# Kernel optimization log

Hardware: AMD Instinct MI355X
Metric: run time of the kernel (lower is better)

Reference implementation:

```python
import jax, jax.numpy as jnp
import numpy as np

L, D, H, F, S, B, P = 6, 1024, 16, 4096, 512, 16, 512
DH = D // H
SCALE = 1.0 / float(np.sqrt(DH))


def setup_inputs() -> dict:
    key = jax.random.key(0)
    ks = jax.random.split(key, 12)
    def n(k, shape, s=0.02):
        return jax.random.normal(k, shape, jnp.float32) * s
    x = jax.random.normal(ks[0], (B, S, D), jnp.float32)
    pe = n(ks[1], (1, P, D))                      # learnable positional encoding
    # per-layer stacked params; linear weights stored [in, out] (y = x @ W + b)
    wq = n(ks[2], (L, D, D)); wk = n(ks[3], (L, D, D)); wv = n(ks[4], (L, D, D))
    wo = n(ks[5], (L, D, D))
    bq = jnp.zeros((L, D)); bk = jnp.zeros((L, D)); bv = jnp.zeros((L, D)); bo = jnp.zeros((L, D))
    bias_table = n(ks[6], (L, 2 * P - 1, H))      # relative position bias table
    w1 = n(ks[7], (L, D, F)); b1 = jnp.zeros((L, F))
    w2 = n(ks[8], (L, F, D)); b2 = jnp.zeros((L, D))
    ln1_g = jnp.ones((L, D)); ln1_b = jnp.zeros((L, D))
    ln2_g = jnp.ones((L, D)); ln2_b = jnp.zeros((L, D))
    return dict(x=x, pe=pe, wq=wq, bq=bq, wk=wk, bk=bk, wv=wv, bv=bv, wo=wo, bo=bo,
                bias_table=bias_table, w1=w1, b1=b1, w2=w2, b2=b2,
                ln1_g=ln1_g, ln1_b=ln1_b, ln2_g=ln2_g, ln2_b=ln2_b)


def _ln(x, g, b):
    mu = jnp.mean(x, -1, keepdims=True)
    var = jnp.mean((x - mu) ** 2, -1, keepdims=True)
    return (x - mu) / jnp.sqrt(var + 1e-6) * g + b


def reference(x, pe, wq, bq, wk, bk, wv, bv, wo, bo, bias_table,
              w1, b1, w2, b2, ln1_g, ln1_b, ln2_g, ln2_b):
    idx = jnp.arange(S)
    rel = idx[:, None] - idx[None, :] + (P - 1)   # [S,S] relative position index
    h = x + pe[:, :S, :]                           # dropout is identity at eval
    for i in range(L):
        xn = _ln(h, ln1_g[i], ln1_b[i])
        q = (xn @ wq[i] + bq[i]).reshape(B, S, H, DH)
        k = (xn @ wk[i] + bk[i]).reshape(B, S, H, DH)
        v = (xn @ wv[i] + bv[i]).reshape(B, S, H, DH)
        scores = jnp.einsum('bqhd,bkhd->bhqk', q, k) * SCALE
        bias = bias_table[i][rel]                  # [S,S,H] gather
        scores = scores + jnp.transpose(bias, (2, 0, 1))[None]  # [1,H,S,S]
        aw = jax.nn.softmax(scores, axis=-1)
        ctx = jnp.einsum('bhqk,bkhd->bqhd', aw, v).reshape(B, S, D)
        attn = ctx @ wo[i] + bo[i]
        out1 = h + attn
        xn2 = _ln(out1, ln2_g[i], ln2_b[i])
        ffn = jax.nn.gelu(xn2 @ w1[i] + b1[i], approximate=False) @ w2[i] + b2[i]
        h = out1 + ffn + h                         # note: double residual, as in source
    return h
```

## Files before the change

### kernel.cpp

```cpp
#include <hip/hip_runtime.h>
#include <cstdint>

typedef unsigned short u16;
typedef __bf16 bf16x8 __attribute__((ext_vector_type(8)));
typedef unsigned short u16x8 __attribute__((ext_vector_type(8)));
typedef float f32x4 __attribute__((ext_vector_type(4)));

__device__ __forceinline__ float b2f(u16 u) { return __uint_as_float(((unsigned)u) << 16); }
__device__ __forceinline__ u16 f2b(float f) {
  unsigned u = __float_as_uint(f);
  return (u16)((u + 0x7FFFu + ((u >> 16) & 1u)) >> 16);
}

#define GLDS(g, l) __builtin_amdgcn_global_load_lds( \
    (const __attribute__((address_space(1))) void*)(g), \
    (__attribute__((address_space(3))) void*)(l), 16, 0, 0)

__global__ __launch_bounds__(256) void addpe_kernel(const float* __restrict__ x,
                                                    const float* __restrict__ pe,
                                                    float* __restrict__ h) {
  int i = blockIdx.x * 256 + threadIdx.x;
  float4 xv = ((const float4*)x)[i];
  float4 pv = ((const float4*)pe)[i & 0x1FFFF];
  float4 o;
  o.x = xv.x + pv.x; o.y = xv.y + pv.y; o.z = xv.z + pv.z; o.w = xv.w + pv.w;
  ((float4*)h)[i] = o;
}

__global__ __launch_bounds__(256) void copy_kernel(const float* __restrict__ h,
                                                   float* __restrict__ out) {
  int i = blockIdx.x * 256 + threadIdx.x;
  ((float4*)out)[i] = ((const float4*)h)[i];
}

__global__ __launch_bounds__(256) void bias_concat_kernel(const float* __restrict__ a,
                                                          const float* __restrict__ b,
                                                          const float* __restrict__ c,
                                                          float* __restrict__ o) {
  int i = blockIdx.x * 256 + threadIdx.x;
  float v = (i < 1024) ? a[i] : ((i < 2048) ? b[i - 1024] : c[i - 2048]);
  o[i] = v;
}

__global__ __launch_bounds__(256) void ln_kernel(const float* __restrict__ in,
                                                 const float* __restrict__ g,
                                                 const float* __restrict__ bta,
                                                 u16* __restrict__ out) {
  int row = blockIdx.x, t = threadIdx.x;
  const float4 v = ((const float4*)(in + (size_t)row * 1024))[t];
  float s = v.x + v.y + v.z + v.w;
  float s2 = v.x * v.x + v.y * v.y + v.z * v.z + v.w * v.w;
#pragma unroll
  for (int off = 32; off > 0; off >>= 1) { s += __shfl_xor(s, off); s2 += __shfl_xor(s2, off); }
  __shared__ __align__(16) float red[8];
  int w = t >> 6;
  if ((t & 63) == 0) { red[w] = s; red[4 + w] = s2; }
  __syncthreads();
  s = red[0] + red[1] + red[2] + red[3];
  s2 = red[4] + red[5] + red[6] + red[7];
  float mu = s * (1.0f / 1024.0f);
  float var = s2 * (1.0f / 1024.0f) - mu * mu;
  float rstd = rsqrtf(var + 1e-6f);
  float4 gv = ((const float4*)g)[t];
  float4 bv = ((const float4*)bta)[t];
  ushort4 o;
  o.x = f2b((v.x - mu) * rstd * gv.x + bv.x);
  o.y = f2b((v.y - mu) * rstd * gv.y + bv.y);
  o.z = f2b((v.z - mu) * rstd * gv.z + bv.z);
  o.w = f2b((v.w - mu) * rstd * gv.w + bv.w);
  ((ushort4*)(out + (size_t)row * 1024))[t] = o;
}

__global__ __launch_bounds__(256) void transpose_kernel(const float* __restrict__ src,
                                                        u16* __restrict__ dst,
                                                        int K, int N) {
  __shared__ __align__(16) float tile[32][33];
  int n0 = blockIdx.x * 32, k0 = blockIdx.y * 32;
  int tx = threadIdx.x, ty = threadIdx.y;
#pragma unroll
  for (int j = 0; j < 4; j++)
    tile[ty + j * 8][tx] = src[(size_t)(k0 + ty + j * 8) * N + n0 + tx];
  __syncthreads();
#pragma unroll
  for (int j = 0; j < 4; j++)
    dst[(size_t)(n0 + ty + j * 8) * K + k0 + tx] = f2b(tile[tx][ty + j * 8]);
}

template <int EPI>
__global__ __launch_bounds__(256) void gemm_bt(const u16* __restrict__ A,
                                               const u16* __restrict__ Wt,
                                               const float* __restrict__ bias,
                                               u16* __restrict__ Cb,
                                               const float* __restrict__ R,
                                               float* __restrict__ F,
                                               int M, int N, int K) {
  __shared__ __align__(16) u16 Asm[128 * 32];
  __shared__ __align__(16) u16 Bsm[128 * 32];
  int t = threadIdx.x;
  int w = t >> 6, lane = t & 63;
  int wm = w >> 1, wn = w & 1;
  int m0 = blockIdx.y * 128, n0 = blockIdx.x * 128;
  int r = t >> 2, c = (t & 3) * 8;
  const u16* Ap = A + (size_t)(m0 + r) * K + c;
  const u16* Bp = Wt + (size_t)(n0 + r) * K + c;
  u16* AsmW = Asm + w * 512;
  u16* BsmW = Bsm + w * 512;
  f32x4 acc[4][4] = {};
  int lrow = lane & 15, kq = (lane >> 4) * 8;
  for (int k0 = 0; k0 < K; k0 += 32) {
    __syncthreads();
    GLDS(Ap, AsmW); GLDS(Ap + (size_t)64 * K, AsmW + 2048);
    GLDS(Bp, BsmW); GLDS(Bp + (size_t)64 * K, BsmW + 2048);
    Ap += 32; Bp += 32;
    __syncthreads();
    bf16x8 af[4], bfr[4];
#pragma unroll
    for (int mi = 0; mi < 4; mi++)
      af[mi] = *(const bf16x8*)(Asm + (wm * 64 + mi * 16 + lrow) * 32 + kq);
#pragma unroll
    for (int ni = 0; ni < 4; ni++)
      bfr[ni] = *(const bf16x8*)(Bsm + (wn * 64 + ni * 16 + lrow) * 32 + kq);
#pragma unroll
    for (int mi = 0; mi < 4; mi++)
#pragma unroll
      for (int ni = 0; ni < 4; ni++)
        acc[mi][ni] = __builtin_amdgcn_mfma_f32_16x16x32_bf16(af[mi], bfr[ni], acc[mi][ni], 0, 0, 0);
  }
  int cm = m0 + wm * 64, cn = n0 + wn * 64;
  int rq = (lane >> 4) * 4, cq = lane & 15;
#pragma unroll
  for (int ni = 0; ni < 4; ni++) {
    int col = cn + ni * 16 + cq;
    float bv = bias[col];
#pragma unroll
    for (int mi = 0; mi < 4; mi++) {
      int row = cm + mi * 16 + rq;
#pragma unroll
      for (int rr = 0; rr < 4; rr++) {
        size_t idx = (size_t)(row + rr) * N + col;
        float v = acc[mi][ni][rr] + bv;
        if constexpr (EPI == 0) {
          Cb[idx] = f2b(v);
        } else if constexpr (EPI == 1) {
          Cb[idx] = f2b(0.5f * v * (1.0f + erff(v * 0.70710678118f)));
        } else if constexpr (EPI == 2) {
          F[idx] = R[idx] + v;
        } else {
          F[idx] = F[idx] + R[idx] + v;
        }
      }
    }
  }
}

template <int EPI>
__global__ __launch_bounds__(512, 2) void gemm256(const u16* __restrict__ A,
                                                  const u16* __restrict__ Wt,
                                                  const float* __restrict__ bias,
                                                  u16* __restrict__ Cb,
                                                  int M, int N, int K) {
  __shared__ __align__(16) u16 As[4 * 8192];
  __shared__ __align__(16) u16 Bs[4 * 8192];
  int t = threadIdx.x;
  int lane = t & 63, w = t >> 6;
  int wm = w >> 2, wn = w & 3;
  int l15 = lane & 15, quad = lane >> 4;
  int m0 = blockIdx.y * 256, n0 = blockIdx.x * 256;

  int swz = 8 * ((t & 3) ^ ((t >> 3) & 3));
  const u16* Ap = A + (size_t)(m0 + (t >> 2)) * K + swz;
  const u16* Bp = Wt + (size_t)(n0 + (t >> 2)) * K + swz;
  u16* AsW = As + t * 8;
  u16* BsW = Bs + t * 8;

  int slotr = 8 * (quad ^ ((l15 >> 1) & 3));
  f32x4 acc[8][4] = {};
  int nt = K >> 5;

#pragma unroll
  for (int pp = 0; pp < 3; ++pp) {
    GLDS(Ap, AsW + pp * 8192);
    GLDS(Ap + (size_t)128 * K, AsW + pp * 8192 + 4096);
    GLDS(Bp, BsW + pp * 8192);
    GLDS(Bp + (size_t)128 * K, BsW + pp * 8192 + 4096);
    Ap += 32; Bp += 32;
  }

  for (int tt = 0; tt < nt; ++tt) {
    if (tt + 2 < nt)      { asm volatile("s_waitcnt vmcnt(8)" : : : "memory"); }
    else if (tt + 1 < nt) { asm volatile("s_waitcnt vmcnt(4)" : : : "memory"); }
    else                  { asm volatile("s_waitcnt vmcnt(0)" : : : "memory"); }
    __builtin_amdgcn_sched_barrier(0);
    __builtin_amdgcn_s_barrier();
    __builtin_amdgcn_sched_barrier(0);
    if (tt + 3 < nt) {
      int bsl = ((tt + 3) & 3) * 8192;
      GLDS(Ap, AsW + bsl);
      GLDS(Ap + (size_t)128 * K, AsW + bsl + 4096);
      GLDS(Bp, BsW + bsl);
      GLDS(Bp + (size_t)128 * K, BsW + bsl + 4096);
      Ap += 32; Bp += 32;
    }
    const u16* Ab = As + (tt & 3) * 8192;
    const u16* Bb = Bs + (tt & 3) * 8192;
    bf16x8 af[8], bfr[4];
#pragma unroll
    for (int mi = 0; mi < 8; mi++)
      af[mi] = *(const bf16x8*)(Ab + (wm * 128 + mi * 16 + l15) * 32 + slotr);
#pragma unroll
    for (int ni = 0; ni < 4; ni++)
      bfr[ni] = *(const bf16x8*)(Bb + (wn * 64 + ni * 16 + l15) * 32 + slotr);
    __builtin_amdgcn_s_setprio(1);
#pragma unroll
    for (int mi = 0; mi < 8; mi++)
#pragma unroll
      for (int ni = 0; ni < 4; ni++)
        acc[mi][ni] = __builtin_amdgcn_mfma_f32_16x16x32_bf16(af[mi], bfr[ni], acc[mi][ni], 0, 0, 0);
    __builtin_amdgcn_s_setprio(0);
  }

  int cm = m0 + wm * 128, cn = n0 + wn * 64;
  int rq = quad * 4, cq = l15;
#pragma unroll
  for (int ni = 0; ni < 4; ni++) {
    int col = cn + ni * 16 + cq;
    float bv = bias[col];
#pragma unroll
    for (int mi = 0; mi < 8; mi++) {
      int row = cm + mi * 16 + rq;
#pragma unroll
      for (int rr = 0; rr < 4; rr++) {
        size_t idx = (size_t)(row + rr) * N + col;
        float v = acc[mi][ni][rr] + bv;
        if constexpr (EPI == 1)
          v = 0.5f * v * (1.0f + erff(v * 0.70710678118f));
        Cb[idx] = f2b(v);
      }
    }
  }
}

__global__ __launch_bounds__(256) void attn_mfma(const u16* __restrict__ Qg,
                                                 const u16* __restrict__ Kg,
                                                 const u16* __restrict__ Vg,
                                                 const float* __restrict__ bt,
                                                 u16* __restrict__ ctx,
                                                 int rs) {
  __shared__ __align__(16) u16 Qs[64 * 72];
  __shared__ __align__(16) u16 Ks[128 * 72];
  __shared__ __align__(16) u16 Vts[64 * 136];
  __shared__ __align__(16) u16 Ps[64 * 136];
  __shared__ __align__(16) u16 bias_s[1023];
  int t = threadIdx.x, w = t >> 6, lane = t & 63;
  int l15 = lane & 15, quad = lane >> 4;
  int q0 = blockIdx.x * 64, h = blockIdx.y, b = blockIdx.z;
  size_t base = ((size_t)b * 512) * rs + (size_t)h * 64;

  {
    int r = t >> 3, c = (t & 7) * 8;
    *(u16x8*)(Qs + r * 72 + c) = *(const u16x8*)(Qg + base + (size_t)(q0 + r) * rs + c);
    *(u16x8*)(Qs + (r + 32) * 72 + c) = *(const u16x8*)(Qg + base + (size_t)(q0 + r + 32) * rs + c);
  }
  for (int e = t; e < 1023; e += 256) bias_s[e] = f2b(bt[e * 16 + h]);

  float m_st[4], l_st[4];
  f32x4 O[4] = {};
#pragma unroll
  for (int i = 0; i < 4; i++) { m_st[i] = -1e30f; l_st[i] = 0.f; }

  __syncthreads();
  bf16x8 aq0 = *(const bf16x8*)(Qs + (w * 16 + l15) * 72 + quad * 8);
  bf16x8 aq1 = *(const bf16x8*)(Qs + (w * 16 + l15) * 72 + 32 + quad * 8);

  for (int kt = 0; kt < 4; kt++) {
    if (kt) __syncthreads();
    {
      int r = t >> 3, c = (t & 7) * 8;
#pragma unroll
      for (int p = 0; p < 4; p++)
        *(u16x8*)(Ks + (p * 32 + r) * 72 + c) =
            *(const u16x8*)(Kg + base + (size_t)(kt * 128 + p * 32 + r) * rs + c);
    }
    {
#pragma unroll
      for (int p = 0; p < 4; p++) {
        u16x8 vv;
        int k8 = kt * 128 + p * 32 + w * 8;
#pragma unroll
        for (int j = 0; j < 8; j++) vv[j] = Vg[base + (size_t)(k8 + j) * rs + lane];
        *(u16x8*)(Vts + lane * 136 + p * 32 + w * 8) = vv;
      }
    }
    __syncthreads();

    f32x4 sc[8];
#pragma unroll
    for (int nt = 0; nt < 8; nt++) {
      bf16x8 bk0 = *(const bf16x8*)(Ks + (nt * 16 + l15) * 72 + quad * 8);
      bf16x8 bk1 = *(const bf16x8*)(Ks + (nt * 16 + l15) * 72 + 32 + quad * 8);
      f32x4 z = {};
      z = __builtin_amdgcn_mfma_f32_16x16x32_bf16(aq0, bk0, z, 0, 0, 0);
      sc[nt] = __builtin_amdgcn_mfma_f32_16x16x32_bf16(aq1, bk1, z, 0, 0, 0);
    }
#pragma unroll
    for (int nt = 0; nt < 8; nt++) {
      int kg = kt * 128 + nt * 16 + l15;
#pragma unroll
      for (int rr = 0; rr < 4; rr++) {
        int qg = q0 + w * 16 + quad * 4 + rr;
        sc[nt][rr] = sc[nt][rr] * 0.125f + b2f(bias_s[qg - kg + 511]);
      }
    }
#pragma unroll
    for (int rr = 0; rr < 4; rr++) {
      float mt = sc[0][rr];
#pragma unroll
      for (int nt = 1; nt < 8; nt++) mt = fmaxf(mt, sc[nt][rr]);
#pragma unroll
      for (int off = 8; off > 0; off >>= 1) mt = fmaxf(mt, __shfl_xor(mt, off));
      float mnew = fmaxf(m_st[rr], mt);
      float alpha = __expf(m_st[rr] - mnew);
      float ps = 0.f;
#pragma unroll
      for (int nt = 0; nt < 8; nt++) {
        float p = __expf(sc[nt][rr] - mnew);
        sc[nt][rr] = p;
        ps += p;
      }
#pragma unroll
      for (int off = 8; off > 0; off >>= 1) ps += __shfl_xor(ps, off);
      m_st[rr] = mnew;
      l_st[rr] = l_st[rr] * alpha + ps;
#pragma unroll
      for (int dt = 0; dt < 4; dt++) O[dt][rr] *= alpha;
#pragma unroll
      for (int nt = 0; nt < 8; nt++)
        Ps[(w * 16 + quad * 4 + rr) * 136 + nt * 16 + l15] = f2b(sc[nt][rr]);
    }
#pragma unroll
    for (int ks = 0; ks < 4; ks++) {
      bf16x8 ap = *(const bf16x8*)(Ps + (w * 16 + l15) * 136 + ks * 32 + quad * 8);
#pragma unroll
      for (int dt = 0; dt < 4; dt++) {
        bf16x8 bv = *(const bf16x8*)(Vts + (dt * 16 + l15) * 136 + ks * 32 + quad * 8);
        O[dt] = __builtin_amdgcn_mfma_f32_16x16x32_bf16(ap, bv, O[dt], 0, 0, 0);
      }
    }
  }
#pragma unroll
  for (int dt = 0; dt < 4; dt++) {
    int col = h * 64 + dt * 16 + l15;
#pragma unroll
    for (int rr = 0; rr < 4; rr++) {
      int row = q0 + w * 16 + quad * 4 + rr;
      ctx[((size_t)b * 512 + row) * 1024 + col] = f2b(O[dt][rr] / l_st[rr]);
    }
  }
}

extern "C" void kernel_launch(void* const* d_in, const int* in_sizes, int n_in,
                              void* d_out, int out_size, void* d_ws, size_t ws_size,
                              hipStream_t stream) {
  (void)in_sizes; (void)n_in; (void)out_size; (void)ws_size;
  const float* x = (const float*)d_in[0];
  const float* pe = (const float*)d_in[1];
  const float* wq = (const float*)d_in[2];
  const float* bq = (const float*)d_in[3];
  const float* wk = (const float*)d_in[4];
  const float* bk = (const float*)d_in[5];
  const float* wv = (const float*)d_in[6];
  const float* bvv = (const float*)d_in[7];
  const float* wo = (const float*)d_in[8];
  const float* bo = (const float*)d_in[9];
  const float* btab = (const float*)d_in[10];
  const float* w1 = (const float*)d_in[11];
  const float* b1 = (const float*)d_in[12];
  const float* w2 = (const float*)d_in[13];
  const float* b2 = (const float*)d_in[14];
  const float* ln1g = (const float*)d_in[15];
  const float* ln1b = (const float*)d_in[16];
  const float* ln2g = (const float*)d_in[17];
  const float* ln2b = (const float*)d_in[18];

  const int M = 8192, D = 1024, F = 4096, NQKV = 3072;
  char* p = (char*)d_ws;
  float* h = (float*)p;   p += (size_t)M * D * 4;
  float* o1 = (float*)p;  p += (size_t)M * D * 4;
  u16* xn = (u16*)p;      p += (size_t)M * D * 2;
  u16* qkv = (u16*)p;     p += (size_t)M * NQKV * 2;
  u16* ctx = (u16*)p;     p += (size_t)M * D * 2;
  u16* mid = qkv;
  u16* wqkvt = (u16*)p;   p += (size_t)NQKV * D * 2;
  u16* wto = (u16*)p;     p += (size_t)D * D * 2;
  u16* wt2 = wqkvt;
  u16* wt1 = (u16*)p;     p += (size_t)D * F * 2;
  float* bqkv = (float*)p; p += (size_t)NQKV * 4;

  addpe_kernel<<<8192, 256, 0, stream>>>(x, pe, h);
  for (int i = 0; i < 6; i++) {
    ln_kernel<<<M, 256, 0, stream>>>(h, ln1g + i * D, ln1b + i * D, xn);
    transpose_kernel<<<dim3(D / 32, D / 32), dim3(32, 8), 0, stream>>>(wq + (size_t)i * D * D, wqkvt, D, D);
    transpose_kernel<<<dim3(D / 32, D / 32), dim3(32, 8), 0, stream>>>(wk + (size_t)i * D * D, wqkvt + (size_t)D * D, D, D);
    transpose_kernel<<<dim3(D / 32, D / 32), dim3(32, 8), 0, stream>>>(wv + (size_t)i * D * D, wqkvt + (size_t)2 * D * D, D, D);
    transpose_kernel<<<dim3(D / 32, D / 32), dim3(32, 8), 0, stream>>>(wo + (size_t)i * D * D, wto, D, D);
    transpose_kernel<<<dim3(F / 32, D / 32), dim3(32, 8), 0, stream>>>(w1 + (size_t)i * D * F, wt1, D, F);
    bias_concat_kernel<<<12, 256, 0, stream>>>(bq + i * D, bk + i * D, bvv + i * D, bqkv);
    gemm256<0><<<dim3(NQKV / 256, M / 256), 512, 0, stream>>>(xn, wqkvt, bqkv, qkv, M, NQKV, D);
    attn_mfma<<<dim3(8, 16, 16), 256, 0, stream>>>(qkv, qkv + D, qkv + 2 * D,
                                                   btab + (size_t)i * 1023 * 16, ctx, NQKV);
    gemm_bt<2><<<dim3(D / 128, M / 128), 256, 0, stream>>>(ctx, wto, bo + i * D, nullptr, h, o1, M, D, D);
    transpose_kernel<<<dim3(D / 32, F / 32), dim3(32, 8), 0, stream>>>(w2 + (size_t)i * F * D, wt2, F, D);
    ln_kernel<<<M, 256, 0, stream>>>(o1, ln2g + i * D, ln2b + i * D, xn);
    gemm256<1><<<dim3(F / 256, M / 256), 512, 0, stream>>>(xn, wt1, b1 + i * F, mid, M, F, D);
    gemm_bt<3><<<dim3(D / 128, M / 128), 256, 0, stream>>>(mid, wt2, b2 + i * D, nullptr, o1, h, M, D, F);
  }
  copy_kernel<<<8192, 256, 0, stream>>>(h, (float*)d_out);
}
```

Measured before the change: 3.232 ms.

## Split GEMM main loop into two phases interleaving LDS reads, prefetch and MFMA

```diff
diff --git a/kernel.cpp b/kernel.cpp
--- a/kernel.cpp
+++ b/kernel.cpp
@@ -185,38 +185,59 @@
     GLDS(Bp + (size_t)128 * K, BsW + pp * 8192 + 4096);
     Ap += 32; Bp += 32;
   }
+  asm volatile("s_waitcnt vmcnt(8)" : : : "memory");
+  __builtin_amdgcn_sched_barrier(0);
+  __builtin_amdgcn_s_barrier();
 
   for (int tt = 0; tt < nt; ++tt) {
-    if (tt + 2 < nt)      { asm volatile("s_waitcnt vmcnt(8)" : : : "memory"); }
-    else if (tt + 1 < nt) { asm volatile("s_waitcnt vmcnt(4)" : : : "memory"); }
-    else                  { asm volatile("s_waitcnt vmcnt(0)" : : : "memory"); }
-    __builtin_amdgcn_sched_barrier(0);
-    __builtin_amdgcn_s_barrier();
-    __builtin_amdgcn_sched_barrier(0);
-    if (tt + 3 < nt) {
-      int bsl = ((tt + 3) & 3) * 8192;
-      GLDS(Ap, AsW + bsl);
-      GLDS(Ap + (size_t)128 * K, AsW + bsl + 4096);
-      GLDS(Bp, BsW + bsl);
-      GLDS(Bp + (size_t)128 * K, BsW + bsl + 4096);
-      Ap += 32; Bp += 32;
-    }
     const u16* Ab = As + (tt & 3) * 8192;
     const u16* Bb = Bs + (tt & 3) * 8192;
-    bf16x8 af[8], bfr[4];
-#pragma unroll
-    for (int mi = 0; mi < 8; mi++)
-      af[mi] = *(const bf16x8*)(Ab + (wm * 128 + mi * 16 + l15) * 32 + slotr);
+    bool pf = (tt + 3 < nt);
+    int bsl = ((tt + 3) & 3) * 8192;
+
+    bf16x8 a0[4], bfr[4];
+#pragma unroll
+    for (int mi = 0; mi < 4; mi++)
+      a0[mi] = *(const bf16x8*)(Ab + (wm * 128 + mi * 16 + l15) * 32 + slotr);
 #pragma unroll
     for (int ni = 0; ni < 4; ni++)
       bfr[ni] = *(const bf16x8*)(Bb + (wn * 64 + ni * 16 + l15) * 32 + slotr);
+    if (pf) { GLDS(Ap, AsW + bsl); GLDS(Ap + (size_t)128 * K, AsW + bsl + 4096); Ap += 32; }
+    __builtin_amdgcn_sched_barrier(0);
+    __builtin_amdgcn_s_barrier();
+    asm volatile("s_waitcnt lgkmcnt(0)" : : : "memory");
+    __builtin_amdgcn_sched_barrier(0);
     __builtin_amdgcn_s_setprio(1);
 #pragma unroll
-    for (int mi = 0; mi < 8; mi++)
+    for (int mi = 0; mi < 4; mi++)
 #pragma unroll
       for (int ni = 0; ni < 4; ni++)
-        acc[mi][ni] = __builtin_amdgcn_mfma_f32_16x16x32_bf16(af[mi], bfr[ni], acc[mi][ni], 0, 0, 0);
+        acc[mi][ni] = __builtin_amdgcn_mfma_f32_16x16x32_bf16(a0[mi], bfr[ni], acc[mi][ni], 0, 0, 0);
     __builtin_amdgcn_s_setprio(0);
+    __builtin_amdgcn_sched_barrier(0);
+    __builtin_amdgcn_s_barrier();
+
+    bf16x8 a1[4];
+#pragma unroll
+    for (int mi = 0; mi < 4; mi++)
+      a1[mi] = *(const bf16x8*)(Ab + (wm * 128 + (mi + 4) * 16 + l15) * 32 + slotr);
+    if (pf) { GLDS(Bp, BsW + bsl); GLDS(Bp + (size_t)128 * K, BsW + bsl + 4096); Bp += 32; }
+    if (tt + 4 <= nt)      { asm volatile("s_waitcnt vmcnt(8)" : : : "memory"); }
+    else if (tt + 3 == nt) { asm volatile("s_waitcnt vmcnt(4)" : : : "memory"); }
+    else if (tt + 2 == nt) { asm volatile("s_waitcnt vmcnt(0)" : : : "memory"); }
+    __builtin_amdgcn_sched_barrier(0);
+    __builtin_amdgcn_s_barrier();
+    asm volatile("s_waitcnt lgkmcnt(0)" : : : "memory");
+    __builtin_amdgcn_sched_barrier(0);
+    __builtin_amdgcn_s_setprio(1);
+#pragma unroll
+    for (int mi = 0; mi < 4; mi++)
+#pragma unroll
+      for (int ni = 0; ni < 4; ni++)
+        acc[mi + 4][ni] = __builtin_amdgcn_mfma_f32_16x16x32_bf16(a1[mi], bfr[ni], acc[mi + 4][ni], 0, 0, 0);
+    __builtin_amdgcn_s_setprio(0);
+    __builtin_amdgcn_sched_barrier(0);
+    __builtin_amdgcn_s_barrier();
   }
 
   int cm = m0 + wm * 128, cn = n0 + wn * 64;
```

Result: faster. 3.090 ms (-4.4%).
